# Performance work log

Hardware: AMD Instinct MI355X
Metric: run time of the kernel (lower is better)

## Reference

```python
import jax, jax.numpy as jnp
import numpy as np

N, F, H, C, E = 100000, 512, 128, 8, 1600000
GAMMA = 1.0
EPS = 1e-8


def _xavier(key, shape):
    a = np.sqrt(6.0 / (shape[0] + shape[1])).astype(np.float32)
    return jax.random.uniform(key, shape, jnp.float32, -a, a)


def _agg(w, x, src, dst):
    # y[i] = sum_{e: dst[e]==i} w[e] * x[src[e]]  (sparse adj @ x)
    return jax.ops.segment_sum(w[:, None] * x[src], dst, num_segments=N)


def setup_inputs() -> dict:
    key = jax.random.key(0)
    ks = jax.random.split(key, 8)
    features = jax.random.normal(ks[0], (N, F), jnp.float32)
    edge_src = jax.random.randint(ks[1], (E,), 0, N)
    edge_dst = jax.random.randint(ks[2], (E,), 0, N)
    # degree-based normalized edge weights, mimicking D^p A D^p
    deg = jnp.zeros((N,), jnp.float32).at[edge_dst].add(1.0)
    deg = jnp.maximum(deg, 1.0)
    d_half = deg ** -0.5
    d_one = deg ** -1.0
    w1 = d_half[edge_dst] * d_half[edge_src]   # D^-1/2 A D^-1/2
    w2 = d_one[edge_dst] * d_one[edge_src]     # D^-1  A D^-1
    Wm1 = _xavier(ks[3], (F, H))
    Ws1 = _xavier(ks[4], (F, H))
    Wm2 = _xavier(ks[5], (H, C))
    Ws2 = _xavier(ks[6], (H, C))
    noise = jax.random.normal(ks[7], (N, C), jnp.float32)
    return {"features": features, "edge_src": edge_src, "edge_dst": edge_dst,
            "w1": w1, "w2": w2, "Wm1": Wm1, "Ws1": Ws1, "Wm2": Wm2,
            "Ws2": Ws2, "noise": noise}


def reference(features, edge_src, edge_dst, w1, w2, Wm1, Ws1, Wm2, Ws2, noise):
    # GGCL_F (eval mode: dropout is identity)
    miu1 = jax.nn.elu(features @ Wm1)
    sigma1 = jax.nn.relu(features @ Ws1)
    att1 = jnp.exp(-GAMMA * sigma1)
    miu_h = _agg(w1, miu1 * att1, edge_src, edge_dst)
    sigma_h = _agg(w2, sigma1 * att1 * att1, edge_src, edge_dst)
    # GGCL_D
    miu2 = jax.nn.elu(miu_h @ Wm2)
    sigma2 = jax.nn.relu(sigma_h @ Ws2)
    att2 = jnp.exp(-GAMMA * sigma2)
    mean_out = _agg(w1, miu2 * att2, edge_src, edge_dst)
    # GGCL_D returns (mean_out, sigma2); reparameterized sample
    return mean_out + noise * jnp.sqrt(sigma2 + EPS)
```

## Files before the change

### kernel.cpp

```cpp
#include <hip/hip_runtime.h>
#include <cstdint>

#define AS1 __attribute__((address_space(1)))
#define AS3 __attribute__((address_space(3)))

typedef __attribute__((ext_vector_type(8))) short short8;
typedef __attribute__((ext_vector_type(4))) float floatx4;
typedef unsigned short u16;

static constexpr int NN   = 100000;
static constexpr int FF   = 512;
static constexpr int HH   = 128;
static constexpr int EE   = 1600000;
static constexpr int PADM = 100096;
static constexpr int NPAD = 100352;
static constexpr int NB   = 98;

__device__ __forceinline__ u16 f2bf_rne(float v) {
    uint32_t u = __builtin_bit_cast(uint32_t, v);
    u += 0x7fffu + ((u >> 16) & 1u);
    return (u16)(u >> 16);
}
__device__ __forceinline__ float bf2f(u16 h) {
    uint32_t u = ((uint32_t)h) << 16;
    return __builtin_bit_cast(float, u);
}
__device__ __forceinline__ void async16(const void* g, void* l) {
    __builtin_amdgcn_global_load_lds((AS1 const void*)g, (AS3 void*)l, 16, 0, 0);
}

__global__ void k_split_w(const float* __restrict__ Wm1, const float* __restrict__ Ws1,
                          u16* __restrict__ whi, u16* __restrict__ wlo) {
    int t = blockIdx.x * 256 + threadIdx.x;
    int n = t >> 9, k = t & 511;
    float v = (n < HH) ? Wm1[k * HH + n] : Ws1[k * HH + (n - HH)];
    u16 h = f2bf_rne(v);
    whi[t] = h;
    wlo[t] = f2bf_rne(v - bf2f(h));
}

__global__ void k_prep_w2(const float* __restrict__ Wm2, const float* __restrict__ Ws2,
                          u16* __restrict__ W2B) {
    int t = blockIdx.x * 256 + threadIdx.x;
    int j = t & 7, l = (t >> 3) & 63, kc = (t >> 9) & 3, p = t >> 11;
    int n = l & 15, quad = l >> 4;
    int k = kc * 32 + quad * 8 + j;
    float v = 0.f;
    if (n < 8) {
        float wv = (p == 0) ? Wm2[k * 8 + n] : Ws2[k * 8 + n];
        v = (p == 2) ? (wv - bf2f(f2bf_rne(wv))) : wv;
    }
    W2B[t] = f2bf_rne(v);
}

__global__ void k_deg(const int* __restrict__ dst, int* __restrict__ deg) {
    int e = blockIdx.x * 256 + threadIdx.x;
    atomicAdd(&deg[dst[e]], 1);
}
__global__ void k_dh(const int* __restrict__ deg, float2* __restrict__ dd) {
    int t = blockIdx.x * 256 + threadIdx.x;
    int d = max(deg[t], 1);
    float df = (float)d;
    dd[t] = make_float2(1.f / sqrtf(df), 1.f / df);
}

__global__ __launch_bounds__(256) void k_gemm(
        const float* __restrict__ A,
        const u16* __restrict__ BhiG, const u16* __restrict__ BloG,
        const u16* __restrict__ W2B, const float2* __restrict__ dd,
        float* __restrict__ Z) {
    __shared__ u16 sm[16384];
    const int tid = threadIdx.x;
    const int w = tid >> 6, lane = tid & 63;
    const int ml = lane & 15, quad = lane >> 4;
    const int rowBase = blockIdx.x * 64;

    floatx4 am[4][2], as_[4][2];
#pragma unroll
    for (int i = 0; i < 4; i++)
#pragma unroll
        for (int j = 0; j < 2; j++) {
            am[i][j]  = (floatx4){0.f, 0.f, 0.f, 0.f};
            as_[i][j] = (floatx4){0.f, 0.f, 0.f, 0.f};
        }

    const int r0 = tid >> 2, ko = (tid & 3) * 8;
    const int arow = min(rowBase + r0, NN - 1);
    const float* gA = A + (size_t)arow * FF + ko;
    const u16* gBh = BhiG + (size_t)r0 * FF + ko;
    const u16* gBl = BloG + (size_t)(128 + r0) * FF + ko;
    const int bdst = 4096 + r0 * 32 + ko;
    const int ldst = 12288 + r0 * 32 + ko;

    const int aoff = ml * 32 + quad * 8;
    const int bmo  = 4096  + (32 * w + ml) * 32 + quad * 8;
    const int bso  = 4096  + (128 + 32 * w + ml) * 32 + quad * 8;
    const int blo_ = 12288 + (32 * w + ml) * 32 + quad * 8;

    for (int kt = 0; kt < FF; kt += 32) {
        __syncthreads();
#pragma unroll
        for (int q = 0; q < 4; q++)
            async16(gBh + (size_t)q * 64 * FF + kt, &sm[bdst + q * 2048]);
#pragma unroll
        for (int q = 0; q < 2; q++)
            async16(gBl + (size_t)q * 64 * FF + kt, &sm[ldst + q * 2048]);
        {
            const float4* pA = (const float4*)(gA + kt);
            float4 x0 = pA[0], x1 = pA[1];
            float xv[8] = {x0.x, x0.y, x0.z, x0.w, x1.x, x1.y, x1.z, x1.w};
            short8 hv, lv;
#pragma unroll
            for (int q = 0; q < 8; q++) {
                u16 hh = f2bf_rne(xv[q]);
                hv[q] = (short)hh;
                lv[q] = (short)f2bf_rne(xv[q] - bf2f(hh));
            }
            *(short8*)&sm[r0 * 32 + ko] = hv;
            *(short8*)&sm[2048 + r0 * 32 + ko] = lv;
        }
        __syncthreads();

        short8 ah[4], al[4];
#pragma unroll
        for (int i = 0; i < 4; i++) ah[i] = *(const short8*)&sm[aoff + i * 512];
#pragma unroll
        for (int i = 0; i < 4; i++) al[i] = *(const short8*)&sm[2048 + aoff + i * 512];
#pragma unroll
        for (int jm = 0; jm < 2; jm++) {
            short8 b = *(const short8*)&sm[bmo + jm * 512];
#pragma unroll
            for (int i = 0; i < 4; i++)
                am[i][jm] = __builtin_amdgcn_mfma_f32_16x16x32_bf16(ah[i], b, am[i][jm], 0, 0, 0);
        }
#pragma unroll
        for (int js = 0; js < 2; js++) {
            short8 bh = *(const short8*)&sm[bso + js * 512];
            short8 bl = *(const short8*)&sm[blo_ + js * 512];
#pragma unroll
            for (int i = 0; i < 4; i++) {
                floatx4 c = as_[i][js];
                c = __builtin_amdgcn_mfma_f32_16x16x32_bf16(ah[i], bh, c, 0, 0, 0);
                c = __builtin_amdgcn_mfma_f32_16x16x32_bf16(ah[i], bl, c, 0, 0, 0);
                c = __builtin_amdgcn_mfma_f32_16x16x32_bf16(al[i], bh, c, 0, 0, 0);
                as_[i][js] = c;
            }
        }
    }

    short8 wm[4], wsh[4], wsl[4];
#pragma unroll
    for (int kc = 0; kc < 4; kc++) {
        wm[kc]  = *(const short8*)&W2B[(kc * 64 + lane) * 8];
        wsh[kc] = *(const short8*)&W2B[2048 + (kc * 64 + lane) * 8];
        wsl[kc] = *(const short8*)&W2B[4096 + (kc * 64 + lane) * 8];
    }
    const int rg = w & 1, pp = w >> 1;

#pragma unroll
    for (int h = 0; h < 2; h++) {
        __syncthreads();
#pragma unroll
        for (int ii = 0; ii < 2; ii++) {
            int i = 2 * h + ii;
#pragma unroll
            for (int jm = 0; jm < 2; jm++) {
                int c = 32 * w + 16 * jm + ml;
#pragma unroll
                for (int r = 0; r < 4; r++) {
                    int lr = ii * 16 + quad * 4 + r;
                    float2 d2 = dd[rowBase + h * 32 + lr];
                    float u = am[i][jm][r], v = as_[i][jm][r];
                    float m1 = u > 0.f ? u : __expf(u) - 1.f;
                    float s1 = v > 0.f ? v : 0.f;
                    float a1 = __expf(-s1);
                    float xmv = d2.x * m1 * a1;
                    float xsv = d2.y * s1 * a1 * a1;
                    u16 hh = f2bf_rne(xsv);
                    sm[lr * 136 + c]        = f2bf_rne(xmv);
                    sm[4352 + lr * 136 + c] = hh;
                    sm[8704 + lr * 136 + c] = f2bf_rne(xsv - bf2f(hh));
                }
            }
        }
        __syncthreads();
        floatx4 z = (floatx4){0.f, 0.f, 0.f, 0.f};
#pragma unroll
        for (int kc = 0; kc < 4; kc++) {
            if (pp == 0) {
                short8 a = *(const short8*)&sm[(rg * 16 + ml) * 136 + kc * 32 + quad * 8];
                z = __builtin_amdgcn_mfma_f32_16x16x32_bf16(a, wm[kc], z, 0, 0, 0);
            } else {
                short8 a = *(const short8*)&sm[4352 + (rg * 16 + ml) * 136 + kc * 32 + quad * 8];
                short8 b = *(const short8*)&sm[8704 + (rg * 16 + ml) * 136 + kc * 32 + quad * 8];
                z = __builtin_amdgcn_mfma_f32_16x16x32_bf16(a, wsh[kc], z, 0, 0, 0);
                z = __builtin_amdgcn_mfma_f32_16x16x32_bf16(a, wsl[kc], z, 0, 0, 0);
                z = __builtin_amdgcn_mfma_f32_16x16x32_bf16(b, wsh[kc], z, 0, 0, 0);
            }
        }
        if (ml < 8) {
            int rowb = rowBase + h * 32 + rg * 16 + quad * 4;
#pragma unroll
            for (int r = 0; r < 4; r++)
                if (rowb + r < NN) Z[(size_t)(rowb + r) * 16 + pp * 8 + ml] = z[r];
        }
    }
}

__global__ void k_scan1(const int* __restrict__ deg, int* __restrict__ bsum) {
    int t = threadIdx.x;
    int4 v = ((const int4*)deg)[blockIdx.x * 256 + t];
    __shared__ int red[256];
    red[t] = v.x + v.y + v.z + v.w;
    __syncthreads();
    for (int o = 128; o > 0; o >>= 1) {
        if (t < o) red[t] += red[t + o];
        __syncthreads();
    }
    if (t == 0) bsum[blockIdx.x] = red[0];
}

__global__ void k_scan2(const int* __restrict__ bsum, int* __restrict__ boff) {
    int t = threadIdx.x;
    __shared__ int s[128];
    int own = (t < NB) ? bsum[t] : 0;
    s[t] = own;
    __syncthreads();
    for (int o = 1; o < 128; o <<= 1) {
        int v = (t >= o) ? s[t - o] : 0;
        __syncthreads();
        s[t] += v;
        __syncthreads();
    }
    if (t < NB) boff[t] = s[t] - own;
}

__global__ void k_scan3(const int* __restrict__ deg, const int* __restrict__ boff,
                        int* __restrict__ ptr, int* __restrict__ cursor) {
    int t = threadIdx.x;
    int gi = blockIdx.x * 256 + t;
    int4 v = ((const int4*)deg)[gi];
    int tsum = v.x + v.y + v.z + v.w;
    __shared__ int s[256];
    s[t] = tsum;
    __syncthreads();
    for (int o = 1; o < 256; o <<= 1) {
        int pv = (t >= o) ? s[t - o] : 0;
        __syncthreads();
        s[t] += pv;
        __syncthreads();
    }
    int base = boff[blockIdx.x] + (s[t] - tsum);
    int4 e;
    e.x = base;
    e.y = base + v.x;
    e.z = e.y + v.y;
    e.w = e.z + v.z;
    ((int4*)ptr)[gi] = e;
    ((int4*)cursor)[gi] = e;
}

__global__ void k_scatter(const int* __restrict__ src, const int* __restrict__ dst,
                          int* __restrict__ cursor, int* __restrict__ pay) {
    int e = blockIdx.x * 256 + threadIdx.x;
    int d = dst[e];
    int p = atomicAdd(&cursor[d], 1);
    int pr = pay[p];
    asm volatile("" :: "v"(pr) : "memory");
    pay[p] = src[e];
}

__global__ __launch_bounds__(256) void k_aggA(const int* __restrict__ ptr,
        const int* __restrict__ pay, const float* __restrict__ Z,
        const float2* __restrict__ dd, float* __restrict__ hm, float* __restrict__ hs) {
    int wave = threadIdx.x >> 6, lane = threadIdx.x & 63;
    int i = blockIdx.x * 4 + wave;
    if (i >= NN) return;
    int er = lane >> 3, c = lane & 7;
    int s0 = ptr[i], e0 = ptr[i + 1];
    float am = 0.f, as_ = 0.f;
    for (int j = s0 + er; j < e0; j += 8) {
        int s = pay[j];
        const float* zr = Z + (size_t)s * 16;
        am  += zr[c];
        as_ += zr[8 + c];
    }
    am  += __shfl_xor(am, 8, 64);
    am  += __shfl_xor(am, 16, 64);
    am  += __shfl_xor(am, 32, 64);
    as_ += __shfl_xor(as_, 8, 64);
    as_ += __shfl_xor(as_, 16, 64);
    as_ += __shfl_xor(as_, 32, 64);
    if (lane < 8) {
        float2 d2 = dd[i];
        hm[i * 8 + lane] = d2.x * am;
        hs[i * 8 + lane] = d2.y * as_;
    }
}

__global__ void k_node(const float* __restrict__ hm, const float* __restrict__ hs,
        const float* __restrict__ noise, const float2* __restrict__ dd,
        float* __restrict__ y, float* __restrict__ out) {
    int t = blockIdx.x * 256 + threadIdx.x;
    float m = hm[t], s = hs[t];
    float miu2 = m > 0.f ? m : __expf(m) - 1.f;
    float s2 = s > 0.f ? s : 0.f;
    y[t] = dd[t >> 3].x * miu2 * __expf(-s2);
    out[t] = noise[t] * sqrtf(s2 + 1e-8f);
}

__global__ __launch_bounds__(256) void k_aggB(const int* __restrict__ ptr,
        const int* __restrict__ pay, const float* __restrict__ y,
        const float2* __restrict__ dd, float* __restrict__ out) {
    int wave = threadIdx.x >> 6, lane = threadIdx.x & 63;
    int i = blockIdx.x * 4 + wave;
    if (i >= NN) return;
    int er = lane >> 3, c = lane & 7;
    int s0 = ptr[i], e0 = ptr[i + 1];
    float acc = 0.f;
    for (int j = s0 + er; j < e0; j += 8) {
        int s = pay[j];
        acc += y[(size_t)s * 8 + c];
    }
    acc += __shfl_xor(acc, 8, 64);
    acc += __shfl_xor(acc, 16, 64);
    acc += __shfl_xor(acc, 32, 64);
    if (lane < 8) out[i * 8 + lane] += dd[i].x * acc;
}

extern "C" void kernel_launch(void* const* d_in, const int* in_sizes, int n_in,
                              void* d_out, int out_size, void* d_ws, size_t ws_size,
                              hipStream_t stream) {
    (void)in_sizes; (void)n_in; (void)out_size; (void)ws_size;
    const float* feat  = (const float*)d_in[0];
    const int*   esrc  = (const int*)d_in[1];
    const int*   edst  = (const int*)d_in[2];
    const float* Wm1   = (const float*)d_in[5];
    const float* Ws1   = (const float*)d_in[6];
    const float* Wm2   = (const float*)d_in[7];
    const float* Ws2   = (const float*)d_in[8];
    const float* noise = (const float*)d_in[9];
    float* out = (float*)d_out;

    char* ws = (char*)d_ws;
    size_t off = 0;
    auto alloc = [&](size_t bytes) -> void* {
        void* p = ws + off;
        off += (bytes + 255) & ~(size_t)255;
        return p;
    };
    u16*    WhiT = (u16*)alloc((size_t)256 * 512 * 2);
    u16*    WloT = (u16*)alloc((size_t)256 * 512 * 2);
    u16*    W2B  = (u16*)alloc((size_t)6144 * 2);
    float*  Z    = (float*)alloc((size_t)NN * 16 * 4);
    float*  hm   = (float*)alloc((size_t)NN * 8 * 4);
    float*  hs   = (float*)alloc((size_t)NN * 8 * 4);
    float*  yb   = (float*)alloc((size_t)NN * 8 * 4);
    int*    deg  = (int*)alloc((size_t)NPAD * 4);
    float2* dd   = (float2*)alloc((size_t)NPAD * 8);
    int*    ptr  = (int*)alloc((size_t)(NPAD + 4) * 4);
    int*    cur  = (int*)alloc((size_t)NPAD * 4);
    int*    bsum = (int*)alloc(256 * 4);
    int*    boff = (int*)alloc(256 * 4);
    int*    pay  = (int*)alloc((size_t)EE * 4);

    hipMemsetAsync(deg, 0, (size_t)NPAD * 4, stream);

    k_deg    <<<EE / 256, 256, 0, stream>>>(edst, deg);
    k_dh     <<<NPAD / 256, 256, 0, stream>>>(deg, dd);
    k_scan1  <<<NB, 256, 0, stream>>>(deg, bsum);
    k_scan2  <<<1, 128, 0, stream>>>(bsum, boff);
    k_scan3  <<<NB, 256, 0, stream>>>(deg, boff, ptr, cur);
    k_scatter<<<EE / 256, 256, 0, stream>>>(esrc, edst, cur, pay);

    k_split_w<<<512, 256, 0, stream>>>(Wm1, Ws1, WhiT, WloT);
    k_prep_w2<<<24, 256, 0, stream>>>(Wm2, Ws2, W2B);
    k_gemm   <<<PADM / 64, 256, 0, stream>>>(feat, WhiT, WloT, W2B, dd, Z);

    k_aggA<<<(NN + 3) / 4, 256, 0, stream>>>(ptr, pay, Z, dd, hm, hs);
    k_node<<<NN * 8 / 256, 256, 0, stream>>>(hm, hs, noise, dd, yb, out);
    k_aggB<<<(NN + 3) / 4, 256, 0, stream>>>(ptr, pay, yb, dd, out);
}
```

Baseline: 600.5 us.

## Double GEMM row tile to 128 with 512 threads, fuse node step, prefetch indices

The first-layer GEMM now runs 512-thread blocks over 128 rows, arranged as a 2x4 wave grid, so each B tile loaded into LDS is reused across twice as many rows. The per-node activation step is folded into the first aggregation kernel, which removes the separate node kernel and the hm/hs round trip through global memory. Both aggregation loops now load the next edge's source index before using the current one, hiding part of the pointer-chasing latency. The costs are more LDS per block (48 KB) and a second-layer epilogue where only half the waves do MFMA work in each phase.

```diff
diff --git a/kernel.cpp b/kernel.cpp
--- a/kernel.cpp
+++ b/kernel.cpp
@@ -64,16 +64,17 @@
     dd[t] = make_float2(1.f / sqrtf(df), 1.f / df);
 }
 
-__global__ __launch_bounds__(256) void k_gemm(
+__global__ __launch_bounds__(512, 4) void k_gemm(
         const float* __restrict__ A,
         const u16* __restrict__ BhiG, const u16* __restrict__ BloG,
         const u16* __restrict__ W2B, const float2* __restrict__ dd,
         float* __restrict__ Z) {
-    __shared__ u16 sm[16384];
+    __shared__ u16 sm[24576];
     const int tid = threadIdx.x;
     const int w = tid >> 6, lane = tid & 63;
     const int ml = lane & 15, quad = lane >> 4;
-    const int rowBase = blockIdx.x * 64;
+    const int wrow = w & 1, wcol = w >> 1;
+    const int rowBase = blockIdx.x * 128;
 
     floatx4 am[4][2], as_[4][2];
 #pragma unroll
@@ -89,22 +90,17 @@
     const float* gA = A + (size_t)arow * FF + ko;
     const u16* gBh = BhiG + (size_t)r0 * FF + ko;
     const u16* gBl = BloG + (size_t)(128 + r0) * FF + ko;
-    const int bdst = 4096 + r0 * 32 + ko;
-    const int ldst = 12288 + r0 * 32 + ko;
-
-    const int aoff = ml * 32 + quad * 8;
-    const int bmo  = 4096  + (32 * w + ml) * 32 + quad * 8;
-    const int bso  = 4096  + (128 + 32 * w + ml) * 32 + quad * 8;
-    const int blo_ = 12288 + (32 * w + ml) * 32 + quad * 8;
+
+    const int aoff = (wrow * 64 + ml) * 32 + quad * 8;
+    const int bmo  = 8192  + (32 * wcol + ml) * 32 + quad * 8;
+    const int bso  = 12288 + (32 * wcol + ml) * 32 + quad * 8;
+    const int blo_ = 16384 + (32 * wcol + ml) * 32 + quad * 8;
 
     for (int kt = 0; kt < FF; kt += 32) {
         __syncthreads();
-#pragma unroll
-        for (int q = 0; q < 4; q++)
-            async16(gBh + (size_t)q * 64 * FF + kt, &sm[bdst + q * 2048]);
-#pragma unroll
-        for (int q = 0; q < 2; q++)
-            async16(gBl + (size_t)q * 64 * FF + kt, &sm[ldst + q * 2048]);
+        async16(gBh + kt,                      &sm[8192  + tid * 8]);
+        async16(gBh + (size_t)128 * FF + kt,   &sm[12288 + tid * 8]);
+        async16(gBl + kt,                      &sm[16384 + tid * 8]);
         {
             const float4* pA = (const float4*)(gA + kt);
             float4 x0 = pA[0], x1 = pA[1];
@@ -116,8 +112,8 @@
                 hv[q] = (short)hh;
                 lv[q] = (short)f2bf_rne(xv[q] - bf2f(hh));
             }
-            *(short8*)&sm[r0 * 32 + ko] = hv;
-            *(short8*)&sm[2048 + r0 * 32 + ko] = lv;
+            *(short8*)&sm[tid * 8] = hv;
+            *(short8*)&sm[4096 + tid * 8] = lv;
         }
         __syncthreads();
 
@@ -125,7 +121,7 @@
 #pragma unroll
         for (int i = 0; i < 4; i++) ah[i] = *(const short8*)&sm[aoff + i * 512];
 #pragma unroll
-        for (int i = 0; i < 4; i++) al[i] = *(const short8*)&sm[2048 + aoff + i * 512];
+        for (int i = 0; i < 4; i++) al[i] = *(const short8*)&sm[4096 + aoff + i * 512];
 #pragma unroll
         for (int jm = 0; jm < 2; jm++) {
             short8 b = *(const short8*)&sm[bmo + jm * 512];
@@ -158,51 +154,55 @@
     const int rg = w & 1, pp = w >> 1;
 
 #pragma unroll
-    for (int h = 0; h < 2; h++) {
-        __syncthreads();
-#pragma unroll
-        for (int ii = 0; ii < 2; ii++) {
-            int i = 2 * h + ii;
-#pragma unroll
-            for (int jm = 0; jm < 2; jm++) {
-                int c = 32 * w + 16 * jm + ml;
-#pragma unroll
-                for (int r = 0; r < 4; r++) {
-                    int lr = ii * 16 + quad * 4 + r;
-                    float2 d2 = dd[rowBase + h * 32 + lr];
-                    float u = am[i][jm][r], v = as_[i][jm][r];
-                    float m1 = u > 0.f ? u : __expf(u) - 1.f;
-                    float s1 = v > 0.f ? v : 0.f;
-                    float a1 = __expf(-s1);
-                    float xmv = d2.x * m1 * a1;
-                    float xsv = d2.y * s1 * a1 * a1;
-                    u16 hh = f2bf_rne(xsv);
-                    sm[lr * 136 + c]        = f2bf_rne(xmv);
-                    sm[4352 + lr * 136 + c] = hh;
-                    sm[8704 + lr * 136 + c] = f2bf_rne(xsv - bf2f(hh));
+    for (int h = 0; h < 4; h++) {
+        __syncthreads();
+        if (wrow == (h >> 1)) {
+#pragma unroll
+            for (int ii = 0; ii < 2; ii++) {
+                int i = (h & 1) * 2 + ii;
+#pragma unroll
+                for (int jm = 0; jm < 2; jm++) {
+                    int c = 32 * wcol + 16 * jm + ml;
+#pragma unroll
+                    for (int r = 0; r < 4; r++) {
+                        int lr = ii * 16 + quad * 4 + r;
+                        float2 d2 = dd[rowBase + h * 32 + lr];
+                        float u = am[i][jm][r], v = as_[i][jm][r];
+                        float m1 = u > 0.f ? u : __expf(u) - 1.f;
+                        float s1 = v > 0.f ? v : 0.f;
+                        float a1 = __expf(-s1);
+                        float xmv = d2.x * m1 * a1;
+                        float xsv = d2.y * s1 * a1 * a1;
+                        u16 hh = f2bf_rne(xsv);
+                        sm[lr * 136 + c]        = f2bf_rne(xmv);
+                        sm[4352 + lr * 136 + c] = hh;
+                        sm[8704 + lr * 136 + c] = f2bf_rne(xsv - bf2f(hh));
+                    }
                 }
             }
         }
         __syncthreads();
-        floatx4 z = (floatx4){0.f, 0.f, 0.f, 0.f};
-#pragma unroll
-        for (int kc = 0; kc < 4; kc++) {
-            if (pp == 0) {
-                short8 a = *(const short8*)&sm[(rg * 16 + ml) * 136 + kc * 32 + quad * 8];
-                z = __builtin_amdgcn_mfma_f32_16x16x32_bf16(a, wm[kc], z, 0, 0, 0);
-            } else {
-                short8 a = *(const short8*)&sm[4352 + (rg * 16 + ml) * 136 + kc * 32 + quad * 8];
-                short8 b = *(const short8*)&sm[8704 + (rg * 16 + ml) * 136 + kc * 32 + quad * 8];
-                z = __builtin_amdgcn_mfma_f32_16x16x32_bf16(a, wsh[kc], z, 0, 0, 0);
-                z = __builtin_amdgcn_mfma_f32_16x16x32_bf16(a, wsl[kc], z, 0, 0, 0);
-                z = __builtin_amdgcn_mfma_f32_16x16x32_bf16(b, wsh[kc], z, 0, 0, 0);
-            }
-        }
-        if (ml < 8) {
-            int rowb = rowBase + h * 32 + rg * 16 + quad * 4;
-#pragma unroll
-            for (int r = 0; r < 4; r++)
-                if (rowb + r < NN) Z[(size_t)(rowb + r) * 16 + pp * 8 + ml] = z[r];
+        if (w < 4) {
+            floatx4 z = (floatx4){0.f, 0.f, 0.f, 0.f};
+#pragma unroll
+            for (int kc = 0; kc < 4; kc++) {
+                if (pp == 0) {
+                    short8 a = *(const short8*)&sm[(rg * 16 + ml) * 136 + kc * 32 + quad * 8];
+                    z = __builtin_amdgcn_mfma_f32_16x16x32_bf16(a, wm[kc], z, 0, 0, 0);
+                } else {
+                    short8 a = *(const short8*)&sm[4352 + (rg * 16 + ml) * 136 + kc * 32 + quad * 8];
+                    short8 b = *(const short8*)&sm[8704 + (rg * 16 + ml) * 136 + kc * 32 + quad * 8];
+                    z = __builtin_amdgcn_mfma_f32_16x16x32_bf16(a, wsh[kc], z, 0, 0, 0);
+                    z = __builtin_amdgcn_mfma_f32_16x16x32_bf16(a, wsl[kc], z, 0, 0, 0);
+                    z = __builtin_amdgcn_mfma_f32_16x16x32_bf16(b, wsh[kc], z, 0, 0, 0);
+                }
+            }
+            if (ml < 8) {
+                int rowb = rowBase + h * 32 + rg * 16 + quad * 4;
+#pragma unroll
+                for (int r = 0; r < 4; r++)
+                    if (rowb + r < NN) Z[(size_t)(rowb + r) * 16 + pp * 8 + ml] = z[r];
+            }
         }
     }
 }
@@ -272,18 +272,24 @@
 
 __global__ __launch_bounds__(256) void k_aggA(const int* __restrict__ ptr,
         const int* __restrict__ pay, const float* __restrict__ Z,
-        const float2* __restrict__ dd, float* __restrict__ hm, float* __restrict__ hs) {
+        const float2* __restrict__ dd, const float* __restrict__ noise,
+        float* __restrict__ y, float* __restrict__ out) {
     int wave = threadIdx.x >> 6, lane = threadIdx.x & 63;
     int i = blockIdx.x * 4 + wave;
     if (i >= NN) return;
     int er = lane >> 3, c = lane & 7;
     int s0 = ptr[i], e0 = ptr[i + 1];
     float am = 0.f, as_ = 0.f;
-    for (int j = s0 + er; j < e0; j += 8) {
-        int s = pay[j];
-        const float* zr = Z + (size_t)s * 16;
+    int j = s0 + er;
+    int sidx = (j < e0) ? pay[j] : -1;
+    while (sidx >= 0) {
+        int jn = j + 8;
+        int snext = (jn < e0) ? pay[jn] : -1;
+        const float* zr = Z + (size_t)sidx * 16;
         am  += zr[c];
         as_ += zr[8 + c];
+        j = jn;
+        sidx = snext;
     }
     am  += __shfl_xor(am, 8, 64);
     am  += __shfl_xor(am, 16, 64);
@@ -293,20 +299,12 @@
     as_ += __shfl_xor(as_, 32, 64);
     if (lane < 8) {
         float2 d2 = dd[i];
-        hm[i * 8 + lane] = d2.x * am;
-        hs[i * 8 + lane] = d2.y * as_;
-    }
-}
-
-__global__ void k_node(const float* __restrict__ hm, const float* __restrict__ hs,
-        const float* __restrict__ noise, const float2* __restrict__ dd,
-        float* __restrict__ y, float* __restrict__ out) {
-    int t = blockIdx.x * 256 + threadIdx.x;
-    float m = hm[t], s = hs[t];
-    float miu2 = m > 0.f ? m : __expf(m) - 1.f;
-    float s2 = s > 0.f ? s : 0.f;
-    y[t] = dd[t >> 3].x * miu2 * __expf(-s2);
-    out[t] = noise[t] * sqrtf(s2 + 1e-8f);
+        float hm = d2.x * am, hs = d2.y * as_;
+        float miu2 = hm > 0.f ? hm : __expf(hm) - 1.f;
+        float s2 = hs > 0.f ? hs : 0.f;
+        y[i * 8 + lane]   = d2.x * miu2 * __expf(-s2);
+        out[i * 8 + lane] = noise[i * 8 + lane] * sqrtf(s2 + 1e-8f);
+    }
 }
 
 __global__ __launch_bounds__(256) void k_aggB(const int* __restrict__ ptr,
@@ -318,9 +316,14 @@
     int er = lane >> 3, c = lane & 7;
     int s0 = ptr[i], e0 = ptr[i + 1];
     float acc = 0.f;
-    for (int j = s0 + er; j < e0; j += 8) {
-        int s = pay[j];
-        acc += y[(size_t)s * 8 + c];
+    int j = s0 + er;
+    int sidx = (j < e0) ? pay[j] : -1;
+    while (sidx >= 0) {
+        int jn = j + 8;
+        int snext = (jn < e0) ? pay[jn] : -1;
+        acc += y[(size_t)sidx * 8 + c];
+        j = jn;
+        sidx = snext;
     }
     acc += __shfl_xor(acc, 8, 64);
     acc += __shfl_xor(acc, 16, 64);
@@ -353,8 +356,6 @@
     u16*    WloT = (u16*)alloc((size_t)256 * 512 * 2);
     u16*    W2B  = (u16*)alloc((size_t)6144 * 2);
     float*  Z    = (float*)alloc((size_t)NN * 16 * 4);
-    float*  hm   = (float*)alloc((size_t)NN * 8 * 4);
-    float*  hs   = (float*)alloc((size_t)NN * 8 * 4);
     float*  yb   = (float*)alloc((size_t)NN * 8 * 4);
     int*    deg  = (int*)alloc((size_t)NPAD * 4);
     float2* dd   = (float2*)alloc((size_t)NPAD * 8);
@@ -375,9 +376,8 @@
 
     k_split_w<<<512, 256, 0, stream>>>(Wm1, Ws1, WhiT, WloT);
     k_prep_w2<<<24, 256, 0, stream>>>(Wm2, Ws2, W2B);
-    k_gemm   <<<PADM / 64, 256, 0, stream>>>(feat, WhiT, WloT, W2B, dd, Z);
-
-    k_aggA<<<(NN + 3) / 4, 256, 0, stream>>>(ptr, pay, Z, dd, hm, hs);
-    k_node<<<NN * 8 / 256, 256, 0, stream>>>(hm, hs, noise, dd, yb, out);
+    k_gemm   <<<PADM / 128, 512, 0, stream>>>(feat, WhiT, WloT, W2B, dd, Z);
+
+    k_aggA<<<(NN + 3) / 4, 256, 0, stream>>>(ptr, pay, Z, dd, noise, yb, out);
     k_aggB<<<(NN + 3) / 4, 256, 0, stream>>>(ptr, pay, yb, dd, out);
 }
```

Result: no change. 597.4 us (-0.5%).
